# Optimization experiments

Hardware: AMD Instinct MI355X
Metric: run time of the kernel (lower is better)

The kernel has to match this reference:

```python
import jax, jax.numpy as jnp
import numpy as np

B, T, H, D = 4, 4096, 1024, 4  # batch, seq_len, hidden_size, max_depth


def setup_inputs() -> dict:
    key = jax.random.key(0)
    ks = jax.random.split(key, 8)
    s = 1.0 / np.sqrt(H)
    x = jax.random.normal(ks[0], (B, T, H), dtype=jnp.float32)
    state = jax.random.normal(ks[1], (B, D, H), dtype=jnp.float32)
    # time_decay_multi initialized as in the torch module: row d = 0.9**(d+1)
    time_decay_multi = jnp.broadcast_to(
        (0.9 ** jnp.arange(1, D + 1, dtype=jnp.float32))[:, None], (D, H)
    ).astype(jnp.float32)
    Wl = jax.random.uniform(ks[2], (D, H), jnp.float32, -s, s)   # level_selector weight [out=D, in=H]
    bl = jax.random.uniform(ks[3], (D,), jnp.float32, -s, s)
    Wv = jax.random.uniform(ks[4], (H, H), jnp.float32, -s, s)
    Wk = jax.random.uniform(ks[5], (H, H), jnp.float32, -s, s)
    Wr = jax.random.uniform(ks[6], (H, H), jnp.float32, -s, s)
    Wo = jax.random.uniform(ks[7], (H, H), jnp.float32, -s, s)
    return {"x": x, "state": state, "time_decay_multi": time_decay_multi,
            "Wl": Wl, "bl": bl, "Wv": Wv, "Wk": Wk, "Wr": Wr, "Wo": Wo}


def reference(x, state, time_decay_multi, Wl, bl, Wv, Wk, Wr, Wo):
    # Projections (torch Linear: y = x @ W.T)
    v = jnp.einsum('bth,oh->bto', x, Wv)
    k = jnp.einsum('bth,oh->bto', x, Wk)
    r = jax.nn.sigmoid(jnp.einsum('bth,oh->bto', x, Wr))
    level_weights = jax.nn.softmax(jnp.einsum('bth,dh->btd', x, Wl) + bl, axis=-1)  # [B,T,D]

    decay = jnp.exp(-jnp.exp(time_decay_multi))        # [D,H]
    decayed_state0 = state * decay[None]               # [B,D,H] (original state is never updated in the loop)
    kv = k * v                                         # [B,T,H]

    # per-step state for depth d is decayed_state0[b,d] + kv[b,t]; weighted sum over depths:
    weighted = (jnp.einsum('btd,bdh->bth', level_weights, decayed_state0)
                + jnp.sum(level_weights, axis=-1, keepdims=True) * kv)  # [B,T,H]
    o = r * weighted
    output = jnp.einsum('bth,oh->bto', o, Wo)

    # new_state after the loop keeps only the LAST timestep contribution
    new_state = decayed_state0 + kv[:, -1][:, None, :]  # [B,D,H]
    return output, new_state
```

## Files before the change

### kernel.cpp

```cpp
#include <hip/hip_runtime.h>

#define B_ 4
#define T_ 4096
#define H_ 1024
#define D_ 4
#define M_ (B_ * T_)
#define OUT_MAIN (M_ * H_)

#define WS_BUF  0UL
#define WS_WK   33554432UL
#define WS_LGW  41943040UL
#define WS_DEC  42205184UL

typedef __bf16 bf16x8 __attribute__((ext_vector_type(8)));
typedef unsigned short u16x4 __attribute__((ext_vector_type(4)));
typedef float f32x4 __attribute__((ext_vector_type(4)));

__device__ __forceinline__ float b2f(unsigned short u) {
    union { unsigned int i; float f; } c;
    c.i = ((unsigned int)u) << 16;
    return c.f;
}
__device__ __forceinline__ unsigned short f2b(float f) {
    union { float f; unsigned int i; } c;
    c.f = f;
    unsigned int x = c.i;
    unsigned int r = (x + 0x7FFFu + ((x >> 16) & 1u)) >> 16;
    return (unsigned short)r;
}

#define BAR()  asm volatile("s_barrier" ::: "memory")
#define GLLDS(gsrc, ldst)                                                     \
    __builtin_amdgcn_global_load_lds(                                         \
        (const __attribute__((address_space(1))) unsigned int*)(gsrc),        \
        (__attribute__((address_space(3))) unsigned int*)(ldst), 16, 0, 0)

__global__ __launch_bounds__(256) void cvtw_k(
    const float* __restrict__ s0, const float* __restrict__ s1,
    const float* __restrict__ s2, const float* __restrict__ s3,
    unsigned short* __restrict__ d)
{
    const int w = blockIdx.y;
    const float* s = (w == 0) ? s0 : (w == 1) ? s1 : (w == 2) ? s2 : s3;
    const int i = blockIdx.x * 256 + threadIdx.x;
    const f32x4 v = ((const f32x4*)s)[i];
    u16x4 o;
    o[0] = f2b(v[0]); o[1] = f2b(v[1]); o[2] = f2b(v[2]); o[3] = f2b(v[3]);
    ((u16x4*)(d + (size_t)w * (H_ * H_)))[i] = o;
}

__global__ __launch_bounds__(256) void logcvt_k(
    const float* __restrict__ X, const float* __restrict__ Wl,
    const float* __restrict__ bl, float* __restrict__ lgw,
    unsigned short* __restrict__ xb)
{
    const int wid  = threadIdx.x >> 6;
    const int lane = threadIdx.x & 63;
    const int row  = blockIdx.x * 4 + wid;
    const float* xp = X + (size_t)row * H_;
    unsigned short* xo = xb + (size_t)row * H_;

    float acc[D_] = {0.f, 0.f, 0.f, 0.f};
    for (int h = lane * 4; h < H_; h += 256) {
        const f32x4 xv = *(const f32x4*)(xp + h);
        u16x4 xc;
        xc[0] = f2b(xv[0]); xc[1] = f2b(xv[1]);
        xc[2] = f2b(xv[2]); xc[3] = f2b(xv[3]);
        *(u16x4*)(xo + h) = xc;
#pragma unroll
        for (int d = 0; d < D_; ++d) {
            const f32x4 wv = *(const f32x4*)(Wl + d * H_ + h);
            acc[d] += xv[0] * wv[0] + xv[1] * wv[1] + xv[2] * wv[2] + xv[3] * wv[3];
        }
    }
#pragma unroll
    for (int off = 32; off; off >>= 1)
#pragma unroll
        for (int d = 0; d < D_; ++d) acc[d] += __shfl_xor(acc[d], off, 64);

    if (lane == 0) {
        float l[D_];
#pragma unroll
        for (int d = 0; d < D_; ++d) l[d] = acc[d] + bl[d];
        const float mx = fmaxf(fmaxf(l[0], l[1]), fmaxf(l[2], l[3]));
        float e[D_], s = 0.f;
#pragma unroll
        for (int d = 0; d < D_; ++d) { e[d] = __expf(l[d] - mx); s += e[d]; }
        const float inv = 1.0f / s;
        f32x4 o;
#pragma unroll
        for (int d = 0; d < D_; ++d) o[d] = e[d] * inv;
        *(f32x4*)(lgw + (size_t)row * 4) = o;
    }
}

__global__ void decstate_k(const float* __restrict__ state,
                           const float* __restrict__ tdm,
                           float* __restrict__ dec)
{
    const int i = blockIdx.x * blockDim.x + threadIdx.x;
    if (i >= B_ * D_ * H_) return;
    const int dh = i & (D_ * H_ - 1);
    dec[i] = state[i] * __expf(-__expf(tdm[dh]));
}

__global__ __launch_bounds__(256) void newstate_k(
    const float* __restrict__ X, const float* __restrict__ Wk,
    const float* __restrict__ Wv, const float* __restrict__ dec,
    float* __restrict__ out2)
{
    const int wid  = threadIdx.x >> 6;
    const int lane = threadIdx.x & 63;
    const int row  = blockIdx.x * 4 + wid;
    const int b    = row >> 10;
    const int h    = row & (H_ - 1);
    const float* xp = X + ((size_t)(b * T_ + (T_ - 1))) * H_;

    float ak = 0.f, av = 0.f;
    for (int j = lane * 4; j < H_; j += 256) {
        const f32x4 xv = *(const f32x4*)(xp + j);
        const f32x4 wk = *(const f32x4*)(Wk + (size_t)h * H_ + j);
        const f32x4 wv = *(const f32x4*)(Wv + (size_t)h * H_ + j);
        ak += xv[0]*wk[0] + xv[1]*wk[1] + xv[2]*wk[2] + xv[3]*wk[3];
        av += xv[0]*wv[0] + xv[1]*wv[1] + xv[2]*wv[2] + xv[3]*wv[3];
    }
#pragma unroll
    for (int off = 32; off; off >>= 1) {
        ak += __shfl_xor(ak, off, 64);
        av += __shfl_xor(av, off, 64);
    }
    if (lane == 0) {
        const float kv = ak * av;
#pragma unroll
        for (int d = 0; d < D_; ++d)
            out2[(size_t)(b * D_ + d) * H_ + h] = dec[(b * D_ + d) * H_ + h] + kv;
    }
}

__global__ __launch_bounds__(512, 2) void gemm_kvr(
    const unsigned short* __restrict__ A,
    const unsigned short* __restrict__ Wk,
    const unsigned short* __restrict__ Wv,
    const unsigned short* __restrict__ Wr,
    unsigned short* __restrict__ Co,
    const float* __restrict__ lgw,
    const float* __restrict__ dec)
{
    __shared__ __align__(16) unsigned short As [2 * 8192];
    __shared__ __align__(16) unsigned short Bks[2 * 8192];
    __shared__ __align__(16) unsigned short Bvs[2 * 8192];
    __shared__ __align__(16) unsigned short Brs[2 * 8192];

    const int tid  = threadIdx.x;
    const int wid  = tid >> 6;
    const int lane = tid & 63;
    const int l15  = lane & 15;
    const int q    = lane >> 4;
    const int wrow = wid >> 2;
    const int wcol = wid & 3;
    const int bcol = blockIdx.x * 128;
    const int brow = blockIdx.y * 128;

    const int g0row = tid >> 3, g0cg = (tid & 7) ^ (g0row & 7);
    const int g1row = 64 + g0row, g1cg = (tid & 7) ^ (g1row & 7);
    const int offA0 = (brow + g0row) * 1024 + g0cg * 8;
    const int offA1 = (brow + g1row) * 1024 + g1cg * 8;
    const int offB0 = (bcol + g0row) * 1024 + g0cg * 8;
    const int offB1 = (bcol + g1row) * 1024 + g1cg * 8;
    const int dst0 = tid * 8;
    const int dst1 = 4096 + tid * 8;

    int gx[2];
#pragma unroll
    for (int ks = 0; ks < 2; ++ks) gx[ks] = ((ks * 4 + q) ^ (l15 & 7)) * 8;
    int aB[4], bB[2];
#pragma unroll
    for (int mi = 0; mi < 4; ++mi) aB[mi] = (wrow * 64 + mi * 16 + l15) * 64;
#pragma unroll
    for (int ni = 0; ni < 2; ++ni) bB[ni] = (wcol * 32 + ni * 16 + l15) * 64;

    f32x4 accK[4][2], accV[4][2], accR[4][2];
#pragma unroll
    for (int i = 0; i < 4; ++i)
#pragma unroll
        for (int j = 0; j < 2; ++j) {
            accK[i][j] = (f32x4){0.f, 0.f, 0.f, 0.f};
            accV[i][j] = (f32x4){0.f, 0.f, 0.f, 0.f};
            accR[i][j] = (f32x4){0.f, 0.f, 0.f, 0.f};
        }

#define SG_A(bo, tau)  do { GLLDS(A  + offA0 + (tau) * 64, As  + (bo) + dst0); \
                            GLLDS(A  + offA1 + (tau) * 64, As  + (bo) + dst1); } while (0)
#define SG_BK(bo, tau) do { GLLDS(Wk + offB0 + (tau) * 64, Bks + (bo) + dst0); \
                            GLLDS(Wk + offB1 + (tau) * 64, Bks + (bo) + dst1); } while (0)
#define SG_BV(bo, tau) do { GLLDS(Wv + offB0 + (tau) * 64, Bvs + (bo) + dst0); \
                            GLLDS(Wv + offB1 + (tau) * 64, Bvs + (bo) + dst1); } while (0)
#define SG_BR(bo, tau) do { GLLDS(Wr + offB0 + (tau) * 64, Brs + (bo) + dst0); \
                            GLLDS(Wr + offB1 + (tau) * 64, Brs + (bo) + dst1); } while (0)
#define RD_AALL(CUR)                                                          \
    _Pragma("unroll") for (int mi = 0; mi < 4; ++mi)                          \
    _Pragma("unroll") for (int ks = 0; ks < 2; ++ks)                          \
        aR[mi][ks] = *(const bf16x8*)&As[(CUR) + aB[mi] + gx[ks]];
#define RD_B(ARR, CUR)                                                        \
    _Pragma("unroll") for (int nj = 0; nj < 2; ++nj)                          \
    _Pragma("unroll") for (int ks = 0; ks < 2; ++ks)                          \
        bR[nj][ks] = *(const bf16x8*)&ARR[(CUR) + bB[nj] + gx[ks]];
#define MFMA16(ACC)                                                           \
    __builtin_amdgcn_s_setprio(1);                                            \
    _Pragma("unroll") for (int mi = 0; mi < 4; ++mi)                          \
    _Pragma("unroll") for (int nj = 0; nj < 2; ++nj)                          \
    _Pragma("unroll") for (int ks = 0; ks < 2; ++ks)                          \
        ACC[mi][nj] = __builtin_amdgcn_mfma_f32_16x16x32_bf16(                \
            aR[mi][ks], bR[nj][ks], ACC[mi][nj], 0, 0, 0);                    \
    __builtin_amdgcn_s_setprio(0);

    SG_A(0, 0); SG_BK(0, 0); SG_BV(0, 0); SG_BR(0, 0);
    asm volatile("s_waitcnt vmcnt(4)" ::: "memory");
    BAR();

#pragma unroll 1
    for (int t = 0; t < 15; ++t) {
        const int cur = (t & 1) << 13;
        const int nxt = cur ^ 8192;
        bf16x8 aR[4][2], bR[2][2];

        RD_AALL(cur); RD_B(Bks, cur);
        SG_A(nxt, t + 1); SG_BK(nxt, t + 1);
        BAR(); MFMA16(accK);
        asm volatile("s_waitcnt vmcnt(6)" ::: "memory");
        BAR();

        RD_B(Bvs, cur);
        SG_BV(nxt, t + 1);
        BAR(); MFMA16(accV);
        asm volatile("s_waitcnt vmcnt(6)" ::: "memory");
        BAR();

        RD_B(Brs, cur);
        SG_BR(nxt, t + 1);
        BAR(); MFMA16(accR);
        asm volatile("s_waitcnt vmcnt(4)" ::: "memory");
        BAR();
    }
    {
        const int cur = 8192;
        bf16x8 aR[4][2], bR[2][2];
        RD_AALL(cur); RD_B(Bks, cur);
        BAR(); MFMA16(accK);
        asm volatile("s_waitcnt vmcnt(2)" ::: "memory");
        BAR();
        RD_B(Bvs, cur);
        BAR(); MFMA16(accV);
        asm volatile("s_waitcnt vmcnt(0)" ::: "memory");
        BAR();
        RD_B(Brs, cur);
        MFMA16(accR);
    }
#undef SG_A
#undef SG_BK
#undef SG_BV
#undef SG_BR
#undef RD_AALL
#undef RD_B
#undef MFMA16

    const int orow0 = brow + wrow * 64;
    const int ocol0 = bcol + wcol * 32;
    const int rbase = q * 4;
    const int b = brow >> 12;
    float dcol[2][4];
#pragma unroll
    for (int ni = 0; ni < 2; ++ni)
#pragma unroll
        for (int d = 0; d < 4; ++d)
            dcol[ni][d] = dec[b * (D_ * H_) + d * H_ + (ocol0 + ni * 16 + l15)];
#pragma unroll
    for (int mi = 0; mi < 4; ++mi)
#pragma unroll
        for (int j = 0; j < 4; ++j) {
            const int r = orow0 + mi * 16 + rbase + j;
            const f32x4 lw = *(const f32x4*)(lgw + (size_t)r * 4);
            const float wsum = lw[0] + lw[1] + lw[2] + lw[3];
#pragma unroll
            for (int ni = 0; ni < 2; ++ni) {
                const size_t idx = (size_t)r * 1024 + (ocol0 + ni * 16 + l15);
                const float kvf = b2f(f2b(accV[mi][ni][j] * b2f(f2b(accK[mi][ni][j]))));
                const float rv  = 1.0f / (1.0f + __expf(-accR[mi][ni][j]));
                const float w   = lw[0] * dcol[ni][0] + lw[1] * dcol[ni][1]
                                + lw[2] * dcol[ni][2] + lw[3] * dcol[ni][3]
                                + wsum * kvf;
                Co[idx] = f2b(rv * w);
            }
        }
}

__global__ __launch_bounds__(512, 2) void gemm_o2(
    const unsigned short* __restrict__ A,
    const unsigned short* __restrict__ Wt,
    float* __restrict__ outf)
{
    __shared__ __align__(16) unsigned short As[2 * 16384];
    __shared__ __align__(16) unsigned short Bs[2 * 8192];

    const int tid  = threadIdx.x;
    const int wid  = tid >> 6;
    const int lane = tid & 63;
    const int l15  = lane & 15;
    const int q    = lane >> 4;
    const int wrow = wid >> 1;
    const int wcol = wid & 1;
    const int brow = blockIdx.x * 256;
    const int bcol = blockIdx.y * 128;

    int offA[4], dstA[4];
#pragma unroll
    for (int i = 0; i < 4; ++i) {
        const int G   = i * 512 + tid;
        const int row = G >> 3;
        const int cg  = (G & 7) ^ (row & 7);
        offA[i] = (brow + row) * 1024 + cg * 8;
        dstA[i] = G * 8;
    }
    int offB[2], dstB[2];
#pragma unroll
    for (int j = 0; j < 2; ++j) {
        const int G   = j * 512 + tid;
        const int row = G >> 3;
        const int cg  = (G & 7) ^ (row & 7);
        offB[j] = (bcol + row) * 1024 + cg * 8;
        dstB[j] = G * 8;
    }

    int gx[2];
#pragma unroll
    for (int ks = 0; ks < 2; ++ks) gx[ks] = ((ks * 4 + q) ^ (l15 & 7)) * 8;
    int aB[4], bB[4];
#pragma unroll
    for (int mi = 0; mi < 4; ++mi) aB[mi] = (wrow * 64 + mi * 16 + l15) * 64;
#pragma unroll
    for (int ni = 0; ni < 4; ++ni) bB[ni] = (wcol * 64 + ni * 16 + l15) * 64;

    f32x4 acc[4][4];
#pragma unroll
    for (int i = 0; i < 4; ++i)
#pragma unroll
        for (int j = 0; j < 4; ++j)
            acc[i][j] = (f32x4){0.f, 0.f, 0.f, 0.f};

#define SG_A(bo, tau)  do { GLLDS(A + offA[0] + (tau) * 64, As + (bo) + dstA[0]); \
                            GLLDS(A + offA[1] + (tau) * 64, As + (bo) + dstA[1]); \
                            GLLDS(A + offA[2] + (tau) * 64, As + (bo) + dstA[2]); \
                            GLLDS(A + offA[3] + (tau) * 64, As + (bo) + dstA[3]); } while (0)
#define SG_B(bo, tau)  do { GLLDS(Wt + offB[0] + (tau) * 64, Bs + (bo) + dstB[0]); \
                            GLLDS(Wt + offB[1] + (tau) * 64, Bs + (bo) + dstB[1]); } while (0)
#define RD_AALL(CUR)                                                          \
    _Pragma("unroll") for (int mi = 0; mi < 4; ++mi)                          \
    _Pragma("unroll") for (int ks = 0; ks < 2; ++ks)                          \
        aR[mi][ks] = *(const bf16x8*)&As[(CUR) + aB[mi] + gx[ks]];
#define RD_B2(CUR, N0)                                                        \
    _Pragma("unroll") for (int nj = 0; nj < 2; ++nj)                          \
    _Pragma("unroll") for (int ks = 0; ks < 2; ++ks)                          \
        bR[nj][ks] = *(const bf16x8*)&Bs[(CUR) + bB[(N0) + nj] + gx[ks]];
#define MFMA16(N0)                                                            \
    __builtin_amdgcn_s_setprio(1);                                            \
    _Pragma("unroll") for (int mi = 0; mi < 4; ++mi)                          \
    _Pragma("unroll") for (int nj = 0; nj < 2; ++nj)                          \
    _Pragma("unroll") for (int ks = 0; ks < 2; ++ks)                          \
        acc[mi][(N0) + nj] = __builtin_amdgcn_mfma_f32_16x16x32_bf16(         \
            aR[mi][ks], bR[nj][ks], acc[mi][(N0) + nj], 0, 0, 0);             \
    __builtin_amdgcn_s_setprio(0);

    SG_A(0, 0); SG_B(0, 0); SG_A(16384, 1);
    asm volatile("s_waitcnt vmcnt(4)" ::: "memory");
    BAR();

#pragma unroll 1
    for (int t = 0; t < 15; ++t) {
        const int curA = (t & 1) << 14;
        const int curB = (t & 1) << 13;
        const int nxtB = curB ^ 8192;
        bf16x8 aR[4][2], bR[2][2];

        RD_AALL(curA); RD_B2(curB, 0);
        SG_B(nxtB, t + 1);
        BAR(); MFMA16(0); BAR();

        RD_B2(curB, 2);
        if (t < 14) SG_A(curA, t + 2);
        BAR(); MFMA16(2);
        if (t < 14) asm volatile("s_waitcnt vmcnt(4)" ::: "memory");
        else        asm volatile("s_waitcnt vmcnt(0)" ::: "memory");
        BAR();
    }
    {
        const int curA = 16384, curB = 8192;
        bf16x8 aR[4][2], bR[2][2];
        RD_AALL(curA);
        RD_B2(curB, 0); MFMA16(0);
        RD_B2(curB, 2); MFMA16(2);
    }
#undef SG_A
#undef SG_B
#undef RD_AALL
#undef RD_B2
#undef MFMA16

    const int orow0 = brow + wrow * 64;
    const int ocol0 = bcol + wcol * 64;
    const int rbase = q * 4;
#pragma unroll
    for (int mi = 0; mi < 4; ++mi)
#pragma unroll
        for (int j = 0; j < 4; ++j) {
            const size_t r = (size_t)(orow0 + mi * 16 + rbase + j);
#pragma unroll
            for (int ni = 0; ni < 4; ++ni)
                outf[r * 1024 + (ocol0 + ni * 16 + l15)] = acc[mi][ni][j];
        }
}

extern "C" void kernel_launch(void* const* d_in, const int* in_sizes, int n_in,
                              void* d_out, int out_size, void* d_ws, size_t ws_size,
                              hipStream_t stream)
{
    const float* x   = (const float*)d_in[0];
    const float* st  = (const float*)d_in[1];
    const float* tdm = (const float*)d_in[2];
    const float* Wl  = (const float*)d_in[3];
    const float* bl  = (const float*)d_in[4];
    const float* Wv  = (const float*)d_in[5];
    const float* Wk  = (const float*)d_in[6];
    const float* Wr  = (const float*)d_in[7];
    const float* Wo  = (const float*)d_in[8];
    float* out = (float*)d_out;

    char* ws = (char*)d_ws;
    unsigned short* buf  = (unsigned short*)(ws + WS_BUF);
    unsigned short* wk_b = (unsigned short*)(ws + WS_WK);
    unsigned short* wv_b = wk_b + 1 * (H_ * H_);
    unsigned short* wr_b = wk_b + 2 * (H_ * H_);
    unsigned short* wo_b = wk_b + 3 * (H_ * H_);
    float* lgw = (float*)(ws + WS_LGW);
    float* dec = (float*)(ws + WS_DEC);

    unsigned short* xb = (unsigned short*)out;

    decstate_k<<<(B_ * D_ * H_ + 255) / 256, 256, 0, stream>>>(st, tdm, dec);
    logcvt_k<<<M_ / 4, 256, 0, stream>>>(x, Wl, bl, lgw, xb);
    newstate_k<<<(B_ * H_) / 4, 256, 0, stream>>>(x, Wk, Wv, dec, out + OUT_MAIN);
    cvtw_k<<<dim3(1024, 4), 256, 0, stream>>>(Wk, Wv, Wr, Wo, wk_b);

    gemm_kvr<<<dim3(H_ / 128, M_ / 128), 512, 0, stream>>>(
        xb, wk_b, wv_b, wr_b, buf, lgw, dec);

    gemm_o2<<<dim3(M_ / 256, H_ / 128), 512, 0, stream>>>(buf, wo_b, out);
}
```

Before: 191.3 us.

## Enlarge output GEMM tile to 256x256 and remap KVR blocks per XCD

The output projection GEMM goes from a 256x128 to a 256x256 block tile. Each block loads B in two halves and splits the MFMA phases into four stages, which raises reuse of A and halves the number of blocks. Separately, the fused K/V/R GEMM remaps its linear block id so consecutive rows of tiles land on the same XCD, aiming for better L2 locality. The cost is more accumulator registers (128 fp32 per thread) and double the LDS for B, which may lower occupancy or cause spills, and the grid shrinks to 256 blocks.

Result: faster. 182.0 us (-4.9%).

```diff
diff --git a/kernel.cpp b/kernel.cpp
--- a/kernel.cpp
+++ b/kernel.cpp
@@ -158,8 +158,12 @@
     const int q    = lane >> 4;
     const int wrow = wid >> 2;
     const int wcol = wid & 3;
-    const int bcol = blockIdx.x * 128;
-    const int brow = blockIdx.y * 128;
+
+    const int lin  = blockIdx.y * 8 + blockIdx.x;
+    const int xcd  = lin & 7;
+    const int slot = lin >> 3;
+    const int brow = (xcd * 16 + (slot >> 3)) * 128;
+    const int bcol = (slot & 7) * 128;
 
     const int g0row = tid >> 3, g0cg = (tid & 7) ^ (g0row & 7);
     const int g1row = 64 + g0row, g1cg = (tid & 7) ^ (g1row & 7);
@@ -294,13 +298,13 @@
         }
 }
 
-__global__ __launch_bounds__(512, 2) void gemm_o2(
+__global__ __launch_bounds__(512, 2) void gemm_o3(
     const unsigned short* __restrict__ A,
     const unsigned short* __restrict__ Wt,
     float* __restrict__ outf)
 {
     __shared__ __align__(16) unsigned short As[2 * 16384];
-    __shared__ __align__(16) unsigned short Bs[2 * 8192];
+    __shared__ __align__(16) unsigned short Bs[2 * 16384];
 
     const int tid  = threadIdx.x;
     const int wid  = tid >> 6;
@@ -310,49 +314,43 @@
     const int wrow = wid >> 1;
     const int wcol = wid & 1;
     const int brow = blockIdx.x * 256;
-    const int bcol = blockIdx.y * 128;
-
-    int offA[4], dstA[4];
+    const int bcol = blockIdx.y * 256;
+
+    int offA[4], offB[4], dstq[4];
 #pragma unroll
     for (int i = 0; i < 4; ++i) {
         const int G   = i * 512 + tid;
         const int row = G >> 3;
         const int cg  = (G & 7) ^ (row & 7);
         offA[i] = (brow + row) * 1024 + cg * 8;
-        dstA[i] = G * 8;
-    }
-    int offB[2], dstB[2];
-#pragma unroll
-    for (int j = 0; j < 2; ++j) {
-        const int G   = j * 512 + tid;
-        const int row = G >> 3;
-        const int cg  = (G & 7) ^ (row & 7);
-        offB[j] = (bcol + row) * 1024 + cg * 8;
-        dstB[j] = G * 8;
+        offB[i] = (bcol + row) * 1024 + cg * 8;
+        dstq[i] = G * 8;
     }
 
     int gx[2];
 #pragma unroll
     for (int ks = 0; ks < 2; ++ks) gx[ks] = ((ks * 4 + q) ^ (l15 & 7)) * 8;
-    int aB[4], bB[4];
+    int aB[4], bB[8];
 #pragma unroll
     for (int mi = 0; mi < 4; ++mi) aB[mi] = (wrow * 64 + mi * 16 + l15) * 64;
 #pragma unroll
-    for (int ni = 0; ni < 4; ++ni) bB[ni] = (wcol * 64 + ni * 16 + l15) * 64;
-
-    f32x4 acc[4][4];
+    for (int ni = 0; ni < 8; ++ni) bB[ni] = (wcol * 128 + ni * 16 + l15) * 64;
+
+    f32x4 acc[4][8];
 #pragma unroll
     for (int i = 0; i < 4; ++i)
 #pragma unroll
-        for (int j = 0; j < 4; ++j)
+        for (int j = 0; j < 8; ++j)
             acc[i][j] = (f32x4){0.f, 0.f, 0.f, 0.f};
 
-#define SG_A(bo, tau)  do { GLLDS(A + offA[0] + (tau) * 64, As + (bo) + dstA[0]); \
-                            GLLDS(A + offA[1] + (tau) * 64, As + (bo) + dstA[1]); \
-                            GLLDS(A + offA[2] + (tau) * 64, As + (bo) + dstA[2]); \
-                            GLLDS(A + offA[3] + (tau) * 64, As + (bo) + dstA[3]); } while (0)
-#define SG_B(bo, tau)  do { GLLDS(Wt + offB[0] + (tau) * 64, Bs + (bo) + dstB[0]); \
-                            GLLDS(Wt + offB[1] + (tau) * 64, Bs + (bo) + dstB[1]); } while (0)
+#define SG_A01(bo, tau) do { GLLDS(A + offA[0] + (tau) * 64, As + (bo) + dstq[0]); \
+                             GLLDS(A + offA[1] + (tau) * 64, As + (bo) + dstq[1]); } while (0)
+#define SG_A23(bo, tau) do { GLLDS(A + offA[2] + (tau) * 64, As + (bo) + dstq[2]); \
+                             GLLDS(A + offA[3] + (tau) * 64, As + (bo) + dstq[3]); } while (0)
+#define SG_BH0(bo, tau) do { GLLDS(Wt + offB[0] + (tau) * 64, Bs + (bo) + dstq[0]); \
+                             GLLDS(Wt + offB[1] + (tau) * 64, Bs + (bo) + dstq[1]); } while (0)
+#define SG_BH1(bo, tau) do { GLLDS(Wt + offB[2] + (tau) * 64, Bs + (bo) + dstq[2]); \
+                             GLLDS(Wt + offB[3] + (tau) * 64, Bs + (bo) + dstq[3]); } while (0)
 #define RD_AALL(CUR)                                                          \
     _Pragma("unroll") for (int mi = 0; mi < 4; ++mi)                          \
     _Pragma("unroll") for (int ks = 0; ks < 2; ++ks)                          \
@@ -370,43 +368,56 @@
             aR[mi][ks], bR[nj][ks], acc[mi][(N0) + nj], 0, 0, 0);             \
     __builtin_amdgcn_s_setprio(0);
 
-    SG_A(0, 0); SG_B(0, 0); SG_A(16384, 1);
+    SG_A01(0, 0); SG_A23(0, 0);
+    SG_BH0(0, 0); SG_BH1(0, 0);
+    SG_A01(16384, 1); SG_A23(16384, 1);
     asm volatile("s_waitcnt vmcnt(4)" ::: "memory");
     BAR();
 
 #pragma unroll 1
     for (int t = 0; t < 15; ++t) {
-        const int curA = (t & 1) << 14;
-        const int curB = (t & 1) << 13;
-        const int nxtB = curB ^ 8192;
+        const int cur = (t & 1) << 14;
+        const int nxt = cur ^ 16384;
         bf16x8 aR[4][2], bR[2][2];
 
-        RD_AALL(curA); RD_B2(curB, 0);
-        SG_B(nxtB, t + 1);
+        RD_AALL(cur); RD_B2(cur, 0);
+        SG_BH0(nxt, t + 1);
         BAR(); MFMA16(0); BAR();
 
-        RD_B2(curB, 2);
-        if (t < 14) SG_A(curA, t + 2);
-        BAR(); MFMA16(2);
+        RD_B2(cur, 2);
+        SG_BH1(nxt, t + 1);
+        BAR(); MFMA16(2); BAR();
+
+        RD_B2(cur, 4);
+        if (t < 14) SG_A01(cur, t + 2);
+        BAR(); MFMA16(4); BAR();
+
+        RD_B2(cur, 6);
+        if (t < 14) SG_A23(cur, t + 2);
+        BAR(); MFMA16(6);
         if (t < 14) asm volatile("s_waitcnt vmcnt(4)" ::: "memory");
         else        asm volatile("s_waitcnt vmcnt(0)" ::: "memory");
         BAR();
     }
     {
-        const int curA = 16384, curB = 8192;
+        const int cur = 16384;
         bf16x8 aR[4][2], bR[2][2];
-        RD_AALL(curA);
-        RD_B2(curB, 0); MFMA16(0);
-        RD_B2(curB, 2); MFMA16(2);
-    }
-#undef SG_A
-#undef SG_B
+        RD_AALL(cur);
+        RD_B2(cur, 0); MFMA16(0);
+        RD_B2(cur, 2); MFMA16(2);
+        RD_B2(cur, 4); MFMA16(4);
+        RD_B2(cur, 6); MFMA16(6);
+    }
+#undef SG_A01
+#undef SG_A23
+#undef SG_BH0
+#undef SG_BH1
 #undef RD_AALL
 #undef RD_B2
 #undef MFMA16
 
     const int orow0 = brow + wrow * 64;
-    const int ocol0 = bcol + wcol * 64;
+    const int ocol0 = bcol + wcol * 128;
     const int rbase = q * 4;
 #pragma unroll
     for (int mi = 0; mi < 4; ++mi)
@@ -414,7 +425,7 @@
         for (int j = 0; j < 4; ++j) {
             const size_t r = (size_t)(orow0 + mi * 16 + rbase + j);
 #pragma unroll
-            for (int ni = 0; ni < 4; ++ni)
+            for (int ni = 0; ni < 8; ++ni)
                 outf[r * 1024 + (ocol0 + ni * 16 + l15)] = acc[mi][ni][j];
         }
 }
@@ -450,8 +461,8 @@
     newstate_k<<<(B_ * H_) / 4, 256, 0, stream>>>(x, Wk, Wv, dec, out + OUT_MAIN);
     cvtw_k<<<dim3(1024, 4), 256, 0, stream>>>(Wk, Wv, Wr, Wo, wk_b);
 
-    gemm_kvr<<<dim3(H_ / 128, M_ / 128), 512, 0, stream>>>(
+    gemm_kvr<<<dim3(8, 128), 512, 0, stream>>>(
         xb, wk_b, wv_b, wr_b, buf, lgw, dec);
 
-    gemm_o2<<<dim3(M_ / 256, H_ / 128), 512, 0, stream>>>(buf, wo_b, out);
-}
+    gemm_o3<<<dim3(M_ / 256, H_ / 256), 512, 0, stream>>>(buf, wo_b, out);
+}
```
